# Performance work log

Hardware: AMD Instinct MI355X
Metric: run time of the kernel (lower is better)

The kernel has to match this reference:

```python
import jax, jax.numpy as jnp
import numpy as np

B, N, D, S = 128, 1024, 512, 64
ITERS = 3
EPS = 1e-8


def setup_inputs() -> dict:
    key = jax.random.key(0)
    ks = jax.random.split(key, 10)
    inp = {
        "inputs_pe": jax.random.normal(ks[0], (B, N, D), dtype=jnp.float32),
        "inputs": jax.random.normal(ks[1], (B, N, D), dtype=jnp.float32),
        "slots": jax.random.normal(ks[2], (1, S, D), dtype=jnp.float32),
        "W1": jax.random.normal(ks[3], (D, D), dtype=jnp.float32) * 0.02,
        "b1": jnp.zeros((D,), dtype=jnp.float32),
        "W2": jax.random.normal(ks[4], (D, D), dtype=jnp.float32) * 0.02,
        "b2": jnp.zeros((D,), dtype=jnp.float32),
        "W3": jax.random.normal(ks[5], (D, D), dtype=jnp.float32) * 0.02,
        "b3": jnp.zeros((D,), dtype=jnp.float32),
    }
    return inp


def reference(inputs_pe, inputs, slots, W1, b1, W2, b2, W3, b3):
    b = inputs_pe.shape[0]
    scale = D ** (-0.5)
    # to_k: Linear -> ReLU -> Linear -> ReLU -> Linear (torch Linear: x @ W.T + b)
    h = jax.nn.relu(jnp.einsum('bnd,ed->bne', inputs_pe, W1) + b1)
    h = jax.nn.relu(jnp.einsum('bnd,ed->bne', h, W2) + b2)
    k = jnp.einsum('bnd,ed->bne', h, W3) + b3  # [b, n, d]

    q = jnp.broadcast_to(slots, (b, S, D))  # slots never updated in the loop
    for _ in range(ITERS):
        dots = jnp.einsum('bid,bjd->bij', q, k) * scale  # [b, S, n]
        s_j = dots.sum(axis=2, keepdims=True)            # sum over keys j -> [b, S, 1]
        s_all = dots.sum(axis=(1, 2), keepdims=True)     # total per batch -> [b, 1, 1]
        dots = dots / s_j * s_all
        attn = jax.nn.sigmoid(dots)
        attn2 = attn / (attn.sum(axis=-1, keepdims=True) + EPS)
        updates = jnp.einsum('bjd,bij->bid', inputs, attn2)  # [b, S, d]
    return updates, attn
```

## Files before the change

### kernel.cpp

```cpp
#include <hip/hip_runtime.h>
#include <stdint.h>

#define Bb 128
#define Nn 1024
#define Dd 512
#define Ss 64

constexpr float kScale = 0.044194173824159216f;
constexpr float kEps = 1e-8f;

typedef __bf16 bf16x8 __attribute__((ext_vector_type(8)));
typedef float f32x4 __attribute__((ext_vector_type(4)));
typedef float f32x16 __attribute__((ext_vector_type(16)));
typedef unsigned short ushort8 __attribute__((ext_vector_type(8)));

#define MFMA32 __builtin_amdgcn_mfma_f32_32x32x16_bf16

__device__ inline unsigned short f2bf_rne(float x) {
  unsigned u = __builtin_bit_cast(unsigned, x);
  u += 0x7FFFu + ((u >> 16) & 1u);
  return (unsigned short)(u >> 16);
}
__device__ inline float bf2f(unsigned short h) {
  unsigned u = ((unsigned)h) << 16;
  return __builtin_bit_cast(float, u);
}

__device__ inline void gl_lds16(const void* g, void* l) {
  typedef unsigned int u32;
  auto gp = (u32 __attribute__((address_space(1)))*)(unsigned long long)(uintptr_t)g;
  auto lp = (u32 __attribute__((address_space(3)))*)(unsigned int)(uintptr_t)l;
  __builtin_amdgcn_global_load_lds(gp, lp, 16, 0, 0);
}

__global__ void cast_split_i(const float* __restrict__ in,
                             unsigned short* __restrict__ out, int n8) {
  int i = blockIdx.x * blockDim.x + threadIdx.x;
  const int stride = gridDim.x * blockDim.x;
  for (; i < n8; i += stride) {
    const float4 v0 = ((const float4*)in)[i * 2];
    const float4 v1 = ((const float4*)in)[i * 2 + 1];
    float f[8] = {v0.x, v0.y, v0.z, v0.w, v1.x, v1.y, v1.z, v1.w};
    ushort8 h, lo;
#pragma unroll
    for (int j = 0; j < 8; j++) {
      h[j] = f2bf_rne(f[j]);
      lo[j] = f2bf_rne(f[j] - bf2f(h[j]));
    }
    ((ushort8*)out)[i * 2] = h;
    ((ushort8*)out)[i * 2 + 1] = lo;
  }
}

template <int ACT>
__global__ __launch_bounds__(512, 1) void gemm_8p(
    const unsigned short* __restrict__ A, const unsigned short* __restrict__ W,
    const float* __restrict__ bias, unsigned short* __restrict__ C) {
  constexpr int NH = 32;
  extern __shared__ unsigned short lds[];
  const int t = threadIdx.x, l = t & 63, w = t >> 6;
  const int wr = w >> 2, wc = w & 3;

  const int wg = ((blockIdx.x & 7) << 7) + (blockIdx.x >> 3);
  const long rowA0 = (long)(wg >> 1) * 256;
  const int colB0 = (wg & 1) * 256;

  const unsigned short* base8 = (w < 4) ? A + rowA0 * 1024 : W + (long)colB0 * 1024;
  const int p2s = ((l >> 1) ^ (l >> 4)) & 1;
  const unsigned short* srcp[4];
  int dstp[4];
#pragma unroll
  for (int j = 0; j < 4; j++) {
    const int cid = (w & 3) * 4 + j;
    srcp[j] = base8 + (long)(cid * 16 + (l >> 2)) * 1024 + p2s * 16 + (l & 1) * 8;
    dstp[j] = (w * 4 + j) * 512;
  }
#define STG(h)                                                            \
  {                                                                       \
    unsigned short* bq_ = lds + ((h) & 3) * 16384;                        \
    _Pragma("unroll") for (int j = 0; j < 4; j++)                         \
        gl_lds16(srcp[j] + (h) * 32, bq_ + dstp[j]);                      \
  }

  const int pp16 = (((l >> 5) ^ ((l >> 2) & 1))) * 16;
  const int abase0 = (wr * 128 + (l & 31)) * 32 + pp16;
  const int bbase0 = 8192 + (wc * 64 + (l & 31)) * 32 + pp16;

  f32x16 acc[4][2] = {};
  bf16x8 ah[4], al[4], bh0, bl0, bh1, bl1;

#define PH_BAR()                                                          \
  __builtin_amdgcn_s_barrier();                                           \
  asm volatile("s_waitcnt lgkmcnt(0)" ::: "memory");                      \
  __builtin_amdgcn_sched_barrier(0);

#define MFMA6(MA, MB, BH, BL)                                             \
  __builtin_amdgcn_s_setprio(1);                                          \
  acc[MA][( &BH == &bh0 ) ? 0 : 1] = acc[MA][(&BH == &bh0) ? 0 : 1];      \
  __builtin_amdgcn_s_setprio(0);


  STG(0); STG(1); STG(2);

  for (int h = 0; h < NH; ++h) {
    if (h < NH - 2) {
      asm volatile("s_waitcnt vmcnt(8)" ::: "memory");
    } else if (h == NH - 2) {
      asm volatile("s_waitcnt vmcnt(4)" ::: "memory");
    } else {
      asm volatile("s_waitcnt vmcnt(0)" ::: "memory");
    }
    __builtin_amdgcn_s_barrier();
    __builtin_amdgcn_sched_barrier(0);
    if (h + 3 < NH) STG(h + 3);
    const unsigned short* bq = lds + (h & 3) * 16384;

    ah[0] = *(const bf16x8*)(bq + abase0);
    al[0] = *(const bf16x8*)(bq + abase0 + 8);
    ah[1] = *(const bf16x8*)(bq + abase0 + 1024);
    al[1] = *(const bf16x8*)(bq + abase0 + 1024 + 8);
    bh0 = *(const bf16x8*)(bq + bbase0);
    bl0 = *(const bf16x8*)(bq + bbase0 + 8);
    PH_BAR()
    __builtin_amdgcn_s_setprio(1);
    acc[0][0] = MFMA32(ah[0], bh0, acc[0][0], 0, 0, 0);
    acc[0][0] = MFMA32(al[0], bh0, acc[0][0], 0, 0, 0);
    acc[0][0] = MFMA32(ah[0], bl0, acc[0][0], 0, 0, 0);
    acc[1][0] = MFMA32(ah[1], bh0, acc[1][0], 0, 0, 0);
    acc[1][0] = MFMA32(al[1], bh0, acc[1][0], 0, 0, 0);
    acc[1][0] = MFMA32(ah[1], bl0, acc[1][0], 0, 0, 0);
    __builtin_amdgcn_s_setprio(0);
    __builtin_amdgcn_sched_barrier(0);

    ah[2] = *(const bf16x8*)(bq + abase0 + 2048);
    al[2] = *(const bf16x8*)(bq + abase0 + 2048 + 8);
    ah[3] = *(const bf16x8*)(bq + abase0 + 3072);
    al[3] = *(const bf16x8*)(bq + abase0 + 3072 + 8);
    PH_BAR()
    __builtin_amdgcn_s_setprio(1);
    acc[2][0] = MFMA32(ah[2], bh0, acc[2][0], 0, 0, 0);
    acc[2][0] = MFMA32(al[2], bh0, acc[2][0], 0, 0, 0);
    acc[2][0] = MFMA32(ah[2], bl0, acc[2][0], 0, 0, 0);
    acc[3][0] = MFMA32(ah[3], bh0, acc[3][0], 0, 0, 0);
    acc[3][0] = MFMA32(al[3], bh0, acc[3][0], 0, 0, 0);
    acc[3][0] = MFMA32(ah[3], bl0, acc[3][0], 0, 0, 0);
    __builtin_amdgcn_s_setprio(0);
    __builtin_amdgcn_sched_barrier(0);

    bh1 = *(const bf16x8*)(bq + bbase0 + 1024);
    bl1 = *(const bf16x8*)(bq + bbase0 + 1024 + 8);
    PH_BAR()
    __builtin_amdgcn_s_setprio(1);
    acc[0][1] = MFMA32(ah[0], bh1, acc[0][1], 0, 0, 0);
    acc[0][1] = MFMA32(al[0], bh1, acc[0][1], 0, 0, 0);
    acc[0][1] = MFMA32(ah[0], bl1, acc[0][1], 0, 0, 0);
    acc[1][1] = MFMA32(ah[1], bh1, acc[1][1], 0, 0, 0);
    acc[1][1] = MFMA32(al[1], bh1, acc[1][1], 0, 0, 0);
    acc[1][1] = MFMA32(ah[1], bl1, acc[1][1], 0, 0, 0);
    __builtin_amdgcn_s_setprio(0);
    __builtin_amdgcn_sched_barrier(0);

    __builtin_amdgcn_s_barrier();
    __builtin_amdgcn_sched_barrier(0);
    __builtin_amdgcn_s_setprio(1);
    acc[2][1] = MFMA32(ah[2], bh1, acc[2][1], 0, 0, 0);
    acc[2][1] = MFMA32(al[2], bh1, acc[2][1], 0, 0, 0);
    acc[2][1] = MFMA32(ah[2], bl1, acc[2][1], 0, 0, 0);
    acc[3][1] = MFMA32(ah[3], bh1, acc[3][1], 0, 0, 0);
    acc[3][1] = MFMA32(al[3], bh1, acc[3][1], 0, 0, 0);
    acc[3][1] = MFMA32(ah[3], bl1, acc[3][1], 0, 0, 0);
    __builtin_amdgcn_s_setprio(0);
    __builtin_amdgcn_sched_barrier(0);
  }
#undef STG
#undef PH_BAR
#undef MFMA6

#pragma unroll
  for (int m = 0; m < 4; m++)
#pragma unroll
    for (int n = 0; n < 2; n++) {
      const int col = colB0 + wc * 64 + n * 32 + (l & 31);
      const float bv = bias[col];
      const int cofs = (col >> 3) * 16 + (col & 7);
#pragma unroll
      for (int r = 0; r < 16; r++) {
        const long row = rowA0 + wr * 128 + m * 32 + (r & 3) + 8 * (r >> 2) + 4 * (l >> 5);
        float xv = acc[m][n][r] + bv;
        if (ACT) xv = fmaxf(xv, 0.0f);
        const unsigned short h = f2bf_rne(xv);
        unsigned short* cp = C + row * 1024 + cofs;
        cp[0] = h;
        cp[8] = f2bf_rne(xv - bf2f(h));
      }
    }
}

__global__ __launch_bounds__(256) void gemm_dots_split(
    const unsigned short* __restrict__ QI, const unsigned short* __restrict__ KI,
    float* __restrict__ dots) {
  constexpr int K = 512, BM = 64, BN = 128, BK = 32;
  __shared__ __align__(16) unsigned short lah[BM * BK];
  __shared__ __align__(16) unsigned short lal[BM * BK];
  __shared__ __align__(16) unsigned short lbh[BN * BK];
  __shared__ __align__(16) unsigned short lbl[BN * BK];
  const int t = threadIdx.x, l = t & 63, w = t >> 6;
  const int b = blockIdx.x >> 3, bc = blockIdx.x & 7;
  const unsigned short* kb = KI + (long)b * Nn * 1024;
  f32x4 acc[4][2] = {};

  const int qbase = (t >> 2) * 1024 + (t & 3) * 16;
  const long kbase0 = (long)(bc * BN + (t >> 2)) * 1024 + (t & 3) * 16;
  const long kbase1 = (long)(bc * BN + 64 + (t >> 2)) * 1024 + (t & 3) * 16;

  for (int k0 = 0; k0 < K; k0 += BK) {
    const int ko = k0 * 2;
    const int lo = w * 512;
    gl_lds16(QI + qbase + ko, lah + lo);
    gl_lds16(QI + qbase + ko + 8, lal + lo);
    gl_lds16(kb + kbase0 + ko, lbh + lo);
    gl_lds16(kb + kbase0 + ko + 8, lbl + lo);
    gl_lds16(kb + kbase1 + ko, lbh + 2048 + lo);
    gl_lds16(kb + kbase1 + ko + 8, lbl + 2048 + lo);
    __syncthreads();
    bf16x8 ah[4], al[4], bh[2], bl[2];
#pragma unroll
    for (int m = 0; m < 4; m++) {
      const int off = (m * 16 + (l & 15)) * BK + (l >> 4) * 8;
      ah[m] = *(const bf16x8*)(lah + off);
      al[m] = *(const bf16x8*)(lal + off);
    }
#pragma unroll
    for (int n = 0; n < 2; n++) {
      const int off = (w * 32 + n * 16 + (l & 15)) * BK + (l >> 4) * 8;
      bh[n] = *(const bf16x8*)(lbh + off);
      bl[n] = *(const bf16x8*)(lbl + off);
    }
#pragma unroll
    for (int m = 0; m < 4; m++)
#pragma unroll
      for (int n = 0; n < 2; n++) {
        acc[m][n] = __builtin_amdgcn_mfma_f32_16x16x32_bf16(ah[m], bh[n], acc[m][n], 0, 0, 0);
        acc[m][n] = __builtin_amdgcn_mfma_f32_16x16x32_bf16(al[m], bh[n], acc[m][n], 0, 0, 0);
        acc[m][n] = __builtin_amdgcn_mfma_f32_16x16x32_bf16(ah[m], bl[n], acc[m][n], 0, 0, 0);
      }
    __syncthreads();
  }
  float* dp = dots + (long)b * Ss * Nn;
#pragma unroll
  for (int m = 0; m < 4; m++) {
    const int row = m * 16 + (l >> 4) * 4;
#pragma unroll
    for (int n = 0; n < 2; n++) {
      const int col = bc * BN + w * 32 + n * 16 + (l & 15);
#pragma unroll
      for (int r = 0; r < 4; r++) dp[(long)(row + r) * Nn + col] = acc[m][n][r] * kScale;
    }
  }
}

__global__ __launch_bounds__(256) void reduce_k(
    const float* __restrict__ dots, float* __restrict__ s_j, float* __restrict__ s_all) {
  const int b = blockIdx.x, t = threadIdx.x, l = t & 63, w = t >> 6;
  const float4* dp = (const float4*)(dots + (long)b * Ss * Nn);
  __shared__ float rowacc[64][4];
  __shared__ float rowsum[64];
  for (int r = 0; r < 64; ++r) {
    const float4 v = dp[r * 256 + t];
    float s = v.x + v.y + v.z + v.w;
#pragma unroll
    for (int off = 32; off; off >>= 1) s += __shfl_down(s, off);
    if (l == 0) rowacc[r][w] = s;
  }
  __syncthreads();
  if (t < 64) {
    const float v = rowacc[t][0] + rowacc[t][1] + rowacc[t][2] + rowacc[t][3];
    rowsum[t] = v;
    s_j[b * 64 + t] = v;
  }
  __syncthreads();
  if (t < 64) {
    float v = rowsum[t];
#pragma unroll
    for (int off = 32; off; off >>= 1) v += __shfl_down(v, off);
    if (t == 0) s_all[b] = v;
  }
}

__global__ __launch_bounds__(256) void attn_k(
    const float* __restrict__ dots, const float* __restrict__ s_j,
    const float* __restrict__ s_all, float* __restrict__ attn_out,
    float* __restrict__ inv_r) {
  const int bi = blockIdx.x;
  const int b = bi >> 6;
  const int t = threadIdx.x;
  const float ratio = s_all[b] / s_j[bi];
  const float* dp = dots + (long)bi * Nn;
  float* ap = attn_out + (long)bi * Nn;
  float s = 0.f;
#pragma unroll
  for (int qq = 0; qq < 4; qq++) {
    const int j = qq * 256 + t;
    const float x = dp[j] * ratio;
    const float a = 1.f / (1.f + expf(-x));
    ap[j] = a;
    s += a;
  }
  __shared__ float red[256];
  red[t] = s;
  __syncthreads();
  for (int off = 128; off > 0; off >>= 1) {
    if (t < off) red[t] += red[t + off];
    __syncthreads();
  }
  if (t == 0) inv_r[bi] = 1.f / (red[0] + kEps);
}

__global__ __launch_bounds__(256, 1) void updates_k2(
    const float* __restrict__ attn, const float* __restrict__ inputs,
    const float* __restrict__ inv_r, float* __restrict__ out0) {
  constexpr int NT2 = 32;
  constexpr int BUF_F = 10240;
  extern __shared__ float ldsf[];
  const int t = threadIdx.x, lam = t & 63, w = t >> 6;
  const int b = blockIdx.x >> 1, dt = blockIdx.x & 1;
  const int ig = t >> 5, dg = t & 31;
  const float* inb = inputs + (size_t)b * (Nn * Dd) + dt * 256;
  const float* attsrc = attn + (size_t)b * (Ss * Nn) + (size_t)(t >> 2) * Nn + (t & 3) * 8;
  float acc[8][8] = {};
  float4 ga0, ga1, gb0, gb1;

#define UISSUE(bufi, tile, G0, G1)                                        \
  {                                                                       \
    const int j0_ = (tile)*32;                                            \
    G0 = *(const float4*)(attsrc + j0_);                                  \
    G1 = *(const float4*)(attsrc + j0_ + 4);                              \
    float* db_ = ldsf + (bufi)*BUF_F;                                     \
    _Pragma("unroll") for (int i_ = 0; i_ < 8; i_++) {                    \
      const int row_ = i_ * 4 + w;                                        \
      gl_lds16(inb + (size_t)(j0_ + row_) * Dd + lam * 4, db_ + row_ * 256); \
    }                                                                     \
  }

#define UWRITE(bufi, G0, G1)                                              \
  {                                                                       \
    float* ab_ = ldsf + (bufi)*BUF_F + 8192;                              \
    const int col_ = t >> 2;                                              \
    const int r0_ = (t & 3) * 8;                                          \
    ab_[(r0_ + 0) * 64 + col_] = G0.x;                                    \
    ab_[(r0_ + 1) * 64 + col_] = G0.y;                                    \
    ab_[(r0_ + 2) * 64 + col_] = G0.z;                                    \
    ab_[(r0_ + 3) * 64 + col_] = G0.w;                                    \
    ab_[(r0_ + 4) * 64 + col_] = G1.x;                                    \
    ab_[(r0_ + 5) * 64 + col_] = G1.y;                                    \
    ab_[(r0_ + 6) * 64 + col_] = G1.z;                                    \
    ab_[(r0_ + 7) * 64 + col_] = G1.w;                                    \
  }

#define UCOMP(bufi)                                                       \
  {                                                                       \
    const float* db_ = ldsf + (bufi)*BUF_F;                               \
    const float* ab_ = db_ + 8192;                                        \
    _Pragma("unroll 4") for (int jj = 0; jj < 32; jj++) {                 \
      float av[8], vv[8];                                                 \
      *(float4*)&av[0] = *(const float4*)(ab_ + jj * 64 + ig * 8);        \
      *(float4*)&av[4] = *(const float4*)(ab_ + jj * 64 + ig * 8 + 4);    \
      *(float4*)&vv[0] = *(const float4*)(db_ + jj * 256 + dg * 8);       \
      *(float4*)&vv[4] = *(const float4*)(db_ + jj * 256 + dg * 8 + 4);   \
      _Pragma("unroll") for (int m_ = 0; m_ < 8; m_++)                    \
          _Pragma("unroll") for (int n_ = 0; n_ < 8; n_++)                \
              acc[m_][n_] = __builtin_fmaf(av[m_], vv[n_], acc[m_][n_]);  \
    }                                                                     \
  }

  UISSUE(0, 0, ga0, ga1);
  UISSUE(1, 1, gb0, gb1);
  UWRITE(0, ga0, ga1);

  for (int tt = 0; tt < NT2; tt += 2) {
    asm volatile("s_waitcnt vmcnt(10)" ::: "memory");
    UWRITE((tt + 1) % 3, gb0, gb1);
    asm volatile("s_waitcnt lgkmcnt(0)" ::: "memory");
    __builtin_amdgcn_s_barrier();
    __builtin_amdgcn_sched_barrier(0);
    if (tt < NT2 - 2) UISSUE((tt + 2) % 3, tt + 2, ga0, ga1);
    UCOMP(tt % 3);
    if (tt + 1 < NT2 - 1) {
      asm volatile("s_waitcnt vmcnt(10)" ::: "memory");
    } else {
      asm volatile("s_waitcnt vmcnt(0)" ::: "memory");
    }
    if (tt + 1 < NT2 - 1) UWRITE((tt + 2) % 3, ga0, ga1);
    asm volatile("s_waitcnt lgkmcnt(0)" ::: "memory");
    __builtin_amdgcn_s_barrier();
    __builtin_amdgcn_sched_barrier(0);
    if (tt + 1 < NT2 - 2) UISSUE((tt + 3) % 3, tt + 3, gb0, gb1);
    UCOMP((tt + 1) % 3);
  }
#undef UISSUE
#undef UWRITE
#undef UCOMP

#pragma unroll
  for (int m = 0; m < 8; m++) {
    const int i = ig * 8 + m;
    const float ir = inv_r[b * 64 + i];
    float4 o0, o1;
    o0.x = acc[m][0] * ir; o0.y = acc[m][1] * ir; o0.z = acc[m][2] * ir; o0.w = acc[m][3] * ir;
    o1.x = acc[m][4] * ir; o1.y = acc[m][5] * ir; o1.z = acc[m][6] * ir; o1.w = acc[m][7] * ir;
    float* op = out0 + (size_t)(b * 64 + i) * Dd + dt * 256 + dg * 8;
    *(float4*)op = o0;
    *(float4*)(op + 4) = o1;
  }
}

extern "C" void kernel_launch(void* const* d_in, const int* in_sizes, int n_in,
                              void* d_out, int out_size, void* d_ws, size_t ws_size,
                              hipStream_t stream) {
  (void)in_sizes; (void)n_in; (void)out_size; (void)ws_size;
  const float* inputs_pe = (const float*)d_in[0];
  const float* inputs = (const float*)d_in[1];
  const float* slots = (const float*)d_in[2];
  const float* W1 = (const float*)d_in[3];
  const float* b1 = (const float*)d_in[4];
  const float* W2 = (const float*)d_in[5];
  const float* b2 = (const float*)d_in[6];
  const float* W3 = (const float*)d_in[7];
  const float* b3 = (const float*)d_in[8];

  char* ws = (char*)d_ws;
  size_t off = 0;
  auto alloc = [&](size_t bytes) -> void* {
    void* p = ws + off;
    off += (bytes + 255) & ~(size_t)255;
    return p;
  };
  const size_t actB = (size_t)Bb * Nn * 1024 * 2;
  unsigned short* AI = (unsigned short*)alloc(actB);
  unsigned short* BI = (unsigned short*)alloc(actB);
  unsigned short* w1i = (unsigned short*)alloc(Dd * 1024 * 2);
  unsigned short* w2i = (unsigned short*)alloc(Dd * 1024 * 2);
  unsigned short* w3i = (unsigned short*)alloc(Dd * 1024 * 2);
  unsigned short* qi = (unsigned short*)alloc(Ss * 1024 * 2);
  float* dotsb = (float*)alloc((size_t)Bb * Ss * Nn * 4);
  float* s_j = (float*)alloc(Bb * Ss * 4);
  float* s_all = (float*)alloc(Bb * 4);
  float* inv_r = (float*)alloc(Bb * Ss * 4);

  float* out_updates = (float*)d_out;
  float* out_attn = out_updates + (size_t)Bb * Ss * Dd;

  const int kLdsG = 4 * 32 * 1024;
  const int kLdsU = 3 * 40 * 1024;
  hipFuncSetAttribute(reinterpret_cast<const void*>(gemm_8p<1>),
                      hipFuncAttributeMaxDynamicSharedMemorySize, kLdsG);
  hipFuncSetAttribute(reinterpret_cast<const void*>(gemm_8p<0>),
                      hipFuncAttributeMaxDynamicSharedMemorySize, kLdsG);
  hipFuncSetAttribute(reinterpret_cast<const void*>(updates_k2),
                      hipFuncAttributeMaxDynamicSharedMemorySize, kLdsU);

  cast_split_i<<<4096, 256, 0, stream>>>(inputs_pe, AI, Bb * Nn * Dd / 8);
  cast_split_i<<<128, 256, 0, stream>>>(W1, w1i, Dd * Dd / 8);
  cast_split_i<<<128, 256, 0, stream>>>(W2, w2i, Dd * Dd / 8);
  cast_split_i<<<128, 256, 0, stream>>>(W3, w3i, Dd * Dd / 8);
  cast_split_i<<<16, 256, 0, stream>>>(slots, qi, Ss * Dd / 8);

  gemm_8p<1><<<1024, 512, kLdsG, stream>>>(AI, w1i, b1, BI);
  gemm_8p<1><<<1024, 512, kLdsG, stream>>>(BI, w2i, b2, AI);
  gemm_8p<0><<<1024, 512, kLdsG, stream>>>(AI, w3i, b3, BI);

  gemm_dots_split<<<Bb * 8, 256, 0, stream>>>(qi, BI, dotsb);
  reduce_k<<<Bb, 256, 0, stream>>>(dotsb, s_j, s_all);
  attn_k<<<Bb * Ss, 256, 0, stream>>>(dotsb, s_j, s_all, out_attn, inv_r);
  updates_k2<<<Bb * 2, 256, kLdsU, stream>>>(out_attn, inputs, inv_r, out_updates);
}
```

Before: 1.054 ms.

## Restructure GEMM mainloop to double-buffered 64-wide K stages with XOR swizzle

The three MLP GEMMs move from a 4-deep ring of 32-element K slices (three stages prefetched, fine-grained vmcnt waits) to two 64-element K stages in double-buffered LDS, halving the number of loop iterations and barriers. The LDS layout changes to an 8-way XOR swizzle over 16-byte chunks so that wider rows stay free of bank conflicts. Each iteration now waits for all outstanding global loads before computing, so there is only one stage of prefetch lookahead, and memory latency may be exposed more than with the deeper ring.

```diff
diff --git a/kernel.cpp b/kernel.cpp
--- a/kernel.cpp
+++ b/kernel.cpp
@@ -53,10 +53,10 @@
 }
 
 template <int ACT>
-__global__ __launch_bounds__(512, 1) void gemm_8p(
+__global__ __launch_bounds__(512, 1) void gemm_g2(
     const unsigned short* __restrict__ A, const unsigned short* __restrict__ W,
     const float* __restrict__ bias, unsigned short* __restrict__ C) {
-  constexpr int NH = 32;
+  constexpr int NS = 16;
   extern __shared__ unsigned short lds[];
   const int t = threadIdx.x, l = t & 63, w = t >> 6;
   const int wr = w >> 2, wc = w & 3;
@@ -66,115 +66,101 @@
   const int colB0 = (wg & 1) * 256;
 
   const unsigned short* base8 = (w < 4) ? A + rowA0 * 1024 : W + (long)colB0 * 1024;
-  const int p2s = ((l >> 1) ^ (l >> 4)) & 1;
-  const unsigned short* srcp[4];
-  int dstp[4];
-#pragma unroll
-  for (int j = 0; j < 4; j++) {
-    const int cid = (w & 3) * 4 + j;
-    srcp[j] = base8 + (long)(cid * 16 + (l >> 2)) * 1024 + p2s * 16 + (l & 1) * 8;
-    dstp[j] = (w * 4 + j) * 512;
-  }
-#define STG(h)                                                            \
+  const int qs = (l & 7) ^ ((l >> 3) & 7);
+  const unsigned short* srcp[8];
+  int dstp[8];
+#pragma unroll
+  for (int j = 0; j < 8; j++) {
+    const int cl = (w & 3) * 8 + j;
+    const int row = cl * 8 + (l >> 3);
+    srcp[j] = base8 + (long)row * 1024 + qs * 8;
+    dstp[j] = (w < 4 ? 0 : 16384) + cl * 512;
+  }
+#define STG(s)                                                            \
   {                                                                       \
-    unsigned short* bq_ = lds + ((h) & 3) * 16384;                        \
-    _Pragma("unroll") for (int j = 0; j < 4; j++)                         \
-        gl_lds16(srcp[j] + (h) * 32, bq_ + dstp[j]);                      \
-  }
-
-  const int pp16 = (((l >> 5) ^ ((l >> 2) & 1))) * 16;
-  const int abase0 = (wr * 128 + (l & 31)) * 32 + pp16;
-  const int bbase0 = 8192 + (wc * 64 + (l & 31)) * 32 + pp16;
+    unsigned short* bq_ = lds + ((s) & 1) * 32768;                        \
+    _Pragma("unroll") for (int j = 0; j < 8; j++)                         \
+        gl_lds16(srcp[j] + (s) * 64, bq_ + dstp[j]);                      \
+  }
+
+  const int p0 = ((2 * (l >> 5)) ^ (l & 7)) * 8;
+  int aoff[4], boff[2];
+#pragma unroll
+  for (int m = 0; m < 4; m++) aoff[m] = (wr * 128 + m * 32 + (l & 31)) * 64 + p0;
+#pragma unroll
+  for (int n = 0; n < 2; n++) boff[n] = 16384 + (wc * 64 + n * 32 + (l & 31)) * 64 + p0;
 
   f32x16 acc[4][2] = {};
   bf16x8 ah[4], al[4], bh0, bl0, bh1, bl1;
 
-#define PH_BAR()                                                          \
+#define PH()                                                              \
   __builtin_amdgcn_s_barrier();                                           \
   asm volatile("s_waitcnt lgkmcnt(0)" ::: "memory");                      \
   __builtin_amdgcn_sched_barrier(0);
 
-#define MFMA6(MA, MB, BH, BL)                                             \
+#define M6(MI, BH, BL, NI)                                                \
   __builtin_amdgcn_s_setprio(1);                                          \
-  acc[MA][( &BH == &bh0 ) ? 0 : 1] = acc[MA][(&BH == &bh0) ? 0 : 1];      \
-  __builtin_amdgcn_s_setprio(0);
-
-
-  STG(0); STG(1); STG(2);
-
-  for (int h = 0; h < NH; ++h) {
-    if (h < NH - 2) {
-      asm volatile("s_waitcnt vmcnt(8)" ::: "memory");
-    } else if (h == NH - 2) {
-      asm volatile("s_waitcnt vmcnt(4)" ::: "memory");
-    } else {
-      asm volatile("s_waitcnt vmcnt(0)" ::: "memory");
-    }
+  acc[MI][NI] = MFMA32(ah[MI], BH, acc[MI][NI], 0, 0, 0);                 \
+  acc[MI][NI] = MFMA32(al[MI], BH, acc[MI][NI], 0, 0, 0);                 \
+  acc[MI][NI] = MFMA32(ah[MI], BL, acc[MI][NI], 0, 0, 0);                 \
+  acc[MI + 1][NI] = MFMA32(ah[MI + 1], BH, acc[MI + 1][NI], 0, 0, 0);     \
+  acc[MI + 1][NI] = MFMA32(al[MI + 1], BH, acc[MI + 1][NI], 0, 0, 0);     \
+  acc[MI + 1][NI] = MFMA32(ah[MI + 1], BL, acc[MI + 1][NI], 0, 0, 0);     \
+  __builtin_amdgcn_s_setprio(0);                                          \
+  __builtin_amdgcn_sched_barrier(0);
+
+  STG(0);
+
+  for (int s = 0; s < NS; ++s) {
+    asm volatile("s_waitcnt vmcnt(0)" ::: "memory");
     __builtin_amdgcn_s_barrier();
     __builtin_amdgcn_sched_barrier(0);
-    if (h + 3 < NH) STG(h + 3);
-    const unsigned short* bq = lds + (h & 3) * 16384;
-
-    ah[0] = *(const bf16x8*)(bq + abase0);
-    al[0] = *(const bf16x8*)(bq + abase0 + 8);
-    ah[1] = *(const bf16x8*)(bq + abase0 + 1024);
-    al[1] = *(const bf16x8*)(bq + abase0 + 1024 + 8);
-    bh0 = *(const bf16x8*)(bq + bbase0);
-    bl0 = *(const bf16x8*)(bq + bbase0 + 8);
-    PH_BAR()
-    __builtin_amdgcn_s_setprio(1);
-    acc[0][0] = MFMA32(ah[0], bh0, acc[0][0], 0, 0, 0);
-    acc[0][0] = MFMA32(al[0], bh0, acc[0][0], 0, 0, 0);
-    acc[0][0] = MFMA32(ah[0], bl0, acc[0][0], 0, 0, 0);
-    acc[1][0] = MFMA32(ah[1], bh0, acc[1][0], 0, 0, 0);
-    acc[1][0] = MFMA32(al[1], bh0, acc[1][0], 0, 0, 0);
-    acc[1][0] = MFMA32(ah[1], bl0, acc[1][0], 0, 0, 0);
-    __builtin_amdgcn_s_setprio(0);
-    __builtin_amdgcn_sched_barrier(0);
-
-    ah[2] = *(const bf16x8*)(bq + abase0 + 2048);
-    al[2] = *(const bf16x8*)(bq + abase0 + 2048 + 8);
-    ah[3] = *(const bf16x8*)(bq + abase0 + 3072);
-    al[3] = *(const bf16x8*)(bq + abase0 + 3072 + 8);
-    PH_BAR()
-    __builtin_amdgcn_s_setprio(1);
-    acc[2][0] = MFMA32(ah[2], bh0, acc[2][0], 0, 0, 0);
-    acc[2][0] = MFMA32(al[2], bh0, acc[2][0], 0, 0, 0);
-    acc[2][0] = MFMA32(ah[2], bl0, acc[2][0], 0, 0, 0);
-    acc[3][0] = MFMA32(ah[3], bh0, acc[3][0], 0, 0, 0);
-    acc[3][0] = MFMA32(al[3], bh0, acc[3][0], 0, 0, 0);
-    acc[3][0] = MFMA32(ah[3], bl0, acc[3][0], 0, 0, 0);
-    __builtin_amdgcn_s_setprio(0);
-    __builtin_amdgcn_sched_barrier(0);
-
-    bh1 = *(const bf16x8*)(bq + bbase0 + 1024);
-    bl1 = *(const bf16x8*)(bq + bbase0 + 1024 + 8);
-    PH_BAR()
-    __builtin_amdgcn_s_setprio(1);
-    acc[0][1] = MFMA32(ah[0], bh1, acc[0][1], 0, 0, 0);
-    acc[0][1] = MFMA32(al[0], bh1, acc[0][1], 0, 0, 0);
-    acc[0][1] = MFMA32(ah[0], bl1, acc[0][1], 0, 0, 0);
-    acc[1][1] = MFMA32(ah[1], bh1, acc[1][1], 0, 0, 0);
-    acc[1][1] = MFMA32(al[1], bh1, acc[1][1], 0, 0, 0);
-    acc[1][1] = MFMA32(ah[1], bl1, acc[1][1], 0, 0, 0);
-    __builtin_amdgcn_s_setprio(0);
-    __builtin_amdgcn_sched_barrier(0);
-
-    __builtin_amdgcn_s_barrier();
-    __builtin_amdgcn_sched_barrier(0);
-    __builtin_amdgcn_s_setprio(1);
-    acc[2][1] = MFMA32(ah[2], bh1, acc[2][1], 0, 0, 0);
-    acc[2][1] = MFMA32(al[2], bh1, acc[2][1], 0, 0, 0);
-    acc[2][1] = MFMA32(ah[2], bl1, acc[2][1], 0, 0, 0);
-    acc[3][1] = MFMA32(ah[3], bh1, acc[3][1], 0, 0, 0);
-    acc[3][1] = MFMA32(al[3], bh1, acc[3][1], 0, 0, 0);
-    acc[3][1] = MFMA32(ah[3], bl1, acc[3][1], 0, 0, 0);
-    __builtin_amdgcn_s_setprio(0);
-    __builtin_amdgcn_sched_barrier(0);
+    if (s + 1 < NS) STG(s + 1);
+    const unsigned short* bq = lds + (s & 1) * 32768;
+
+    ah[0] = *(const bf16x8*)(bq + aoff[0]);
+    al[0] = *(const bf16x8*)(bq + (aoff[0] ^ 8));
+    ah[1] = *(const bf16x8*)(bq + aoff[1]);
+    al[1] = *(const bf16x8*)(bq + (aoff[1] ^ 8));
+    bh0 = *(const bf16x8*)(bq + boff[0]);
+    bl0 = *(const bf16x8*)(bq + (boff[0] ^ 8));
+    PH()
+    M6(0, bh0, bl0, 0)
+    ah[2] = *(const bf16x8*)(bq + aoff[2]);
+    al[2] = *(const bf16x8*)(bq + (aoff[2] ^ 8));
+    ah[3] = *(const bf16x8*)(bq + aoff[3]);
+    al[3] = *(const bf16x8*)(bq + (aoff[3] ^ 8));
+    PH()
+    M6(2, bh0, bl0, 0)
+    bh1 = *(const bf16x8*)(bq + boff[1]);
+    bl1 = *(const bf16x8*)(bq + (boff[1] ^ 8));
+    PH()
+    M6(0, bh1, bl1, 1)
+    ah[0] = *(const bf16x8*)(bq + (aoff[0] ^ 32));
+    al[0] = *(const bf16x8*)(bq + (aoff[0] ^ 40));
+    ah[1] = *(const bf16x8*)(bq + (aoff[1] ^ 32));
+    al[1] = *(const bf16x8*)(bq + (aoff[1] ^ 40));
+    bh0 = *(const bf16x8*)(bq + (boff[0] ^ 32));
+    bl0 = *(const bf16x8*)(bq + (boff[0] ^ 40));
+    PH()
+    M6(2, bh1, bl1, 1)
+    ah[2] = *(const bf16x8*)(bq + (aoff[2] ^ 32));
+    al[2] = *(const bf16x8*)(bq + (aoff[2] ^ 40));
+    ah[3] = *(const bf16x8*)(bq + (aoff[3] ^ 32));
+    al[3] = *(const bf16x8*)(bq + (aoff[3] ^ 40));
+    PH()
+    M6(0, bh0, bl0, 0)
+    bh1 = *(const bf16x8*)(bq + (boff[1] ^ 32));
+    bl1 = *(const bf16x8*)(bq + (boff[1] ^ 40));
+    PH()
+    M6(2, bh0, bl0, 0)
+    PH()
+    M6(0, bh1, bl1, 1)
+    M6(2, bh1, bl1, 1)
   }
 #undef STG
-#undef PH_BAR
-#undef MFMA6
+#undef PH
+#undef M6
 
 #pragma unroll
   for (int m = 0; m < 4; m++)
@@ -450,11 +436,11 @@
   float* out_updates = (float*)d_out;
   float* out_attn = out_updates + (size_t)Bb * Ss * Dd;
 
-  const int kLdsG = 4 * 32 * 1024;
+  const int kLdsG = 2 * 64 * 1024;
   const int kLdsU = 3 * 40 * 1024;
-  hipFuncSetAttribute(reinterpret_cast<const void*>(gemm_8p<1>),
+  hipFuncSetAttribute(reinterpret_cast<const void*>(gemm_g2<1>),
                       hipFuncAttributeMaxDynamicSharedMemorySize, kLdsG);
-  hipFuncSetAttribute(reinterpret_cast<const void*>(gemm_8p<0>),
+  hipFuncSetAttribute(reinterpret_cast<const void*>(gemm_g2<0>),
                       hipFuncAttributeMaxDynamicSharedMemorySize, kLdsG);
   hipFuncSetAttribute(reinterpret_cast<const void*>(updates_k2),
                       hipFuncAttributeMaxDynamicSharedMemorySize, kLdsU);
@@ -465,9 +451,9 @@
   cast_split_i<<<128, 256, 0, stream>>>(W3, w3i, Dd * Dd / 8);
   cast_split_i<<<16, 256, 0, stream>>>(slots, qi, Ss * Dd / 8);
 
-  gemm_8p<1><<<1024, 512, kLdsG, stream>>>(AI, w1i, b1, BI);
-  gemm_8p<1><<<1024, 512, kLdsG, stream>>>(BI, w2i, b2, AI);
-  gemm_8p<0><<<1024, 512, kLdsG, stream>>>(AI, w3i, b3, BI);
+  gemm_g2<1><<<1024, 512, kLdsG, stream>>>(AI, w1i, b1, BI);
+  gemm_g2<1><<<1024, 512, kLdsG, stream>>>(BI, w2i, b2, AI);
+  gemm_g2<0><<<1024, 512, kLdsG, stream>>>(AI, w3i, b3, BI);
 
   gemm_dots_split<<<Bb * 8, 256, 0, stream>>>(qi, BI, dotsb);
   reduce_k<<<Bb, 256, 0, stream>>>(dotsb, s_j, s_all);
```

New measurement: 1.040 ms. Within noise of the previous version (-1.3%).
